# Kernel optimization log

Hardware: AMD Instinct MI355X
Metric: run time of the kernel (lower is better)

Reference implementation:

```python
import jax, jax.numpy as jnp
import numpy as np

N_NODES = 100000
N_EMBED = 64
N_HIDDEN = 64
N_EDGES = 1200000


def setup_inputs() -> dict:
    key = jax.random.key(0)
    ks = jax.random.split(key, 8)
    prop_edge_index = jax.random.randint(ks[0], (2, N_EDGES), 0, N_NODES, dtype=jnp.int64)
    emb = jax.random.normal(ks[1], (N_NODES, N_EMBED), dtype=jnp.float32) * 0.05
    # ChebConv K=2 -> two linear weights per layer + bias
    W1_0 = jax.random.normal(ks[2], (N_EMBED, N_HIDDEN), dtype=jnp.float32) * 0.05
    W1_1 = jax.random.normal(ks[3], (N_EMBED, N_HIDDEN), dtype=jnp.float32) * 0.05
    b1 = jnp.zeros((N_HIDDEN,), dtype=jnp.float32)
    W2_0 = jax.random.normal(ks[4], (N_HIDDEN, N_HIDDEN), dtype=jnp.float32) * 0.05
    W2_1 = jax.random.normal(ks[5], (N_HIDDEN, N_HIDDEN), dtype=jnp.float32) * 0.05
    b2 = jnp.zeros((N_HIDDEN,), dtype=jnp.float32)
    return {"prop_edge_index": prop_edge_index, "emb": emb,
            "W1_0": W1_0, "W1_1": W1_1, "b1": b1,
            "W2_0": W2_0, "W2_1": W2_1, "b2": b2}


def _cheb_norm(edge_index, num_nodes):
    """PyG ChebConv.__norm__ with sym normalization, lambda_max=2.0.
    L_hat = 2L/lambda_max - I = (I - D^-1/2 A D^-1/2) - I, so the net
    diagonal weight is 0 and off-diagonal weight is -d_i^-1/2 * d_j^-1/2.
    Self loops in the input are removed first (weight 0)."""
    row, col = edge_index[0], edge_index[1]
    w = jnp.where(row != col, 1.0, 0.0).astype(jnp.float32)  # remove_self_loops
    deg = jax.ops.segment_sum(w, row, num_segments=num_nodes)
    dinv = jnp.where(deg > 0, deg ** -0.5, 0.0)
    norm = -dinv[row] * w * dinv[col]
    return norm


def _cheb_conv(x, src, dst, norm, W0, W1, b, num_nodes):
    # K=2: out = T0(x) @ W0 + T1(x) @ W1 + b, T0 = x, T1 = L_hat x
    Tx1 = jax.ops.segment_sum(norm[:, None] * x[src], dst, num_segments=num_nodes)
    return x @ W0 + Tx1 @ W1 + b


def reference(prop_edge_index, emb, W1_0, W1_1, b1, W2_0, W2_1, b2):
    src, dst = prop_edge_index[0], prop_edge_index[1]
    norm = _cheb_norm(prop_edge_index, N_NODES)
    x = _cheb_conv(emb, src, dst, norm, W1_0, W1_1, b1, N_NODES)
    x = jax.nn.relu(x)
    # dropout: eval mode (identity)
    x = _cheb_conv(x, src, dst, norm, W2_0, W2_1, b2, N_NODES)
    return x
```

## Files before the change

### kernel.cpp

```cpp
#include <hip/hip_runtime.h>

#define N_NODES 100000
#define N_EDGES 1200000
#define NF 64

typedef __attribute__((ext_vector_type(8))) short short8;
typedef __attribute__((ext_vector_type(4))) float float4v;

__device__ __forceinline__ ushort f2bf(float f) {
    unsigned u = __float_as_uint(f);
    return (ushort)((u + 0x7FFF + ((u >> 16) & 1)) >> 16);
}

#define NBINS 391
#define CAP 4352
#define EPB 2048
#define NBLK 586
#define NI4 (N_EDGES / 4)

#define OFF_CNT    0
#define OFF_ENDP   400128
#define OFF_DINV   800256
#define OFF_CUR    1200384
#define OFF_PKW    1203584
#define OFF_SRCS   1236352
#define OFF_SBIN   8042880
#define OFF_DBIN   11446144
#define OFF_EMBBF  18252672
#define OFF_HBF    31052672

__global__ __launch_bounds__(256) void prepsort(const float* __restrict__ W10,
                                                const float* __restrict__ W11,
                                                const float* __restrict__ W20,
                                                const float* __restrict__ W21,
                                                ushort* __restrict__ pk,
                                                const float* __restrict__ emb,
                                                ushort* __restrict__ emb_bf,
                                                const int* __restrict__ row,
                                                const int* __restrict__ col,
                                                int* __restrict__ cur,
                                                ushort* __restrict__ sbinned,
                                                int* __restrict__ dbinned) {
    int b = blockIdx.x;
    int t = threadIdx.x;
    if (b < NBLK) {
        __shared__ int sh[NBINS], dh[NBINS];
        __shared__ int sbase[NBINS], dbase[NBINS];
        for (int i = t; i < NBINS; i += 256) { sh[i] = 0; dh[i] = 0; }
        __syncthreads();
        int i40 = (b * (EPB / 4)) + t * 2;
        int4 r0 = make_int4(-1, -1, -1, -1), c0 = r0, r1 = r0, c1 = r0;
        if (i40 < NI4)     { r0 = ((const int4*)row)[i40];     c0 = ((const int4*)col)[i40]; }
        if (i40 + 1 < NI4) { r1 = ((const int4*)row)[i40 + 1]; c1 = ((const int4*)col)[i40 + 1]; }
        int s_[8] = {r0.x, r0.y, r0.z, r0.w, r1.x, r1.y, r1.z, r1.w};
        int d_[8] = {c0.x, c0.y, c0.z, c0.w, c1.x, c1.y, c1.z, c1.w};
#pragma unroll
        for (int j = 0; j < 8; ++j)
            if (s_[j] >= 0 && s_[j] != d_[j]) {
                atomicAdd(&sh[s_[j] >> 8], 1);
                atomicAdd(&dh[d_[j] >> 8], 1);
            }
        __syncthreads();
        for (int i = t; i < NBINS; i += 256) {
            if (sh[i]) sbase[i] = i * CAP + atomicAdd(&cur[i], sh[i]);
            if (dh[i]) dbase[i] = i * CAP + atomicAdd(&cur[NBINS + i], dh[i]);
        }
        __syncthreads();
#pragma unroll
        for (int j = 0; j < 8; ++j) {
            int s = s_[j], d = d_[j];
            if (s >= 0 && s != d) {
                int ss = atomicAdd(&sbase[s >> 8], 1);
                sbinned[ss] = (ushort)(s & 255);
                int ds = atomicAdd(&dbase[d >> 8], 1);
                dbinned[ds] = (s << 8) | (d & 255);
            }
        }
    } else if (b < NBLK + 8) {
        int idx = (b - NBLK) * 256 + t;
        int layer = idx >> 10;
        int rest = idx & 1023;
        int f = rest >> 6, L = rest & 63;
        int n = (f & 3) * 16 + (L & 15);
        int kb = (f >> 2) * 32 + ((L >> 4) << 3);
#pragma unroll
        for (int j = 0; j < 8; ++j) {
            int k = kb + j;
            const float* W = layer ? ((k < 64) ? W20 : W21) : ((k < 64) ? W10 : W11);
            pk[idx * 8 + j] = f2bf(W[(k & 63) * 64 + n]);
        }
    } else {
        int bb = b - NBLK - 8;
        int i = (bb * 256 + t) * 8;
        float4 v0 = *(const float4*)(emb + i);
        float4 v1 = *(const float4*)(emb + i + 4);
        uint4 o;
        o.x = (uint)f2bf(v0.x) | ((uint)f2bf(v0.y) << 16);
        o.y = (uint)f2bf(v0.z) | ((uint)f2bf(v0.w) << 16);
        o.z = (uint)f2bf(v1.x) | ((uint)f2bf(v1.y) << 16);
        o.w = (uint)f2bf(v1.z) | ((uint)f2bf(v1.w) << 16);
        *(uint4*)(emb_bf + i) = o;
    }
}

__global__ __launch_bounds__(256) void build(const ushort* __restrict__ sbinned,
                                             const int* __restrict__ dbinned,
                                             const int* __restrict__ cur,
                                             float* __restrict__ dinv,
                                             int* __restrict__ cnt,
                                             int* __restrict__ endp,
                                             int* __restrict__ srcs) {
    int t = threadIdx.x;
    int b = blockIdx.x;
    if (b < NBINS) {
        __shared__ int hist[256];
        hist[t] = 0;
        __syncthreads();
        int start = b * CAP;
        int end = start + cur[b];
        for (int i = start + t; i < end; i += 256)
            atomicAdd(&hist[sbinned[i]], 1);
        __syncthreads();
        int n0 = (b << 8) + t;
        if (n0 < N_NODES) dinv[n0] = hist[t] ? rsqrtf((float)hist[t]) : 0.0f;
    } else {
        int bb = b - NBINS;
        __shared__ int ecache[CAP];
        __shared__ int hist[256];
        __shared__ int lcur[256];
        __shared__ int tot_s;
        hist[t] = 0;
        __syncthreads();
        int start = bb * CAP;
        int len = cur[NBINS + bb];
        for (int i = t; i < len; i += 256) {
            int p = dbinned[start + i];
            ecache[i] = p;
            atomicAdd(&hist[p & 255], 1);
        }
        __syncthreads();
        int o0 = hist[t];
        int A0 = (o0 + 3) & ~3;
        __syncthreads();
        hist[t] = A0;
        __syncthreads();
        for (int off = 1; off < 256; off <<= 1) {
            int v = (t >= off) ? hist[t - off] : 0;
            __syncthreads();
            hist[t] += v;
            __syncthreads();
        }
        int e0 = hist[t] - A0;
        if (t == 255) tot_s = hist[255];
        lcur[t] = start + e0;
        int n0 = (bb << 8) + t;
        if (n0 < N_NODES) { cnt[n0] = o0; endp[n0] = start + e0 + o0; }
        __syncthreads();
        for (int i = t; i < len; i += 256) {
            int p = ecache[i];
            int slot = atomicAdd(&lcur[p & 255], 1);
            srcs[slot] = p >> 8;
        }
        __syncthreads();
        for (int k = o0; k < A0; ++k) srcs[start + e0 + k] = 0;
        if (t < 16) srcs[start + tot_s + t] = 0;
    }
}

#define NPW 16
#define WPB 2
#define NPB (NPW * WPB)
#define LB2 ((N_NODES + NPB - 1) / NPB)

__global__ __launch_bounds__(128, 8) void cheb_layer(const ushort* __restrict__ x,
                                                     const int* __restrict__ srcs,
                                                     const float* __restrict__ dinv,
                                                     const int* __restrict__ endp,
                                                     const int* __restrict__ cnt,
                                                     const ushort* __restrict__ pk,
                                                     const float* __restrict__ bias,
                                                     ushort* __restrict__ out_bf,
                                                     float* __restrict__ out_f32,
                                                     int last) {
    __shared__ ushort sA[WPB][16][136];

    int t = threadIdx.x;
    int lane = t & 63, wid = t >> 6;
    int c = lane & 15, q = lane >> 4;
    int qd = q, fg = c;
    int nb = blockIdx.x * NPB + wid * NPW;

    int nend = 0, ncnt = 0;
    if (lane < NPW && nb + lane < N_NODES) {
        nend = endp[nb + lane];
        ncnt = cnt[nb + lane];
    }

    const uint2* xr = (const uint2*)x;

    auto chunk8 = [&](int eb, int eendL, float& a0, float& a1, float& a2, float& a3) {
        int4 sv = *(const int4*)(srcs + eb);
        int4 sw = *(const int4*)(srcs + eb + 4);
        int sA01 = (qd & 1) ? sv.y : sv.x;
        int sA23 = (qd & 1) ? sv.w : sv.z;
        int srcA = (qd & 2) ? sA23 : sA01;
        int sB01 = (qd & 1) ? sw.y : sw.x;
        int sB23 = (qd & 1) ? sw.w : sw.z;
        int srcB = (qd & 2) ? sB23 : sB01;
        float nAf = dinv[srcA];
        float nBf = dinv[srcB];
        nAf = (eb + qd < eendL) ? nAf : 0.0f;
        nBf = (eb + 4 + qd < eendL) ? nBf : 0.0f;
        uint2 gA = xr[(size_t)srcA * 16 + fg];
        uint2 gB = xr[(size_t)srcB * 16 + fg];
        a0 = fmaf(nAf, __uint_as_float(gA.x << 16), a0);
        a1 = fmaf(nAf, __uint_as_float(gA.x & 0xffff0000u), a1);
        a2 = fmaf(nAf, __uint_as_float(gA.y << 16), a2);
        a3 = fmaf(nAf, __uint_as_float(gA.y & 0xffff0000u), a3);
        a0 = fmaf(nBf, __uint_as_float(gB.x << 16), a0);
        a1 = fmaf(nBf, __uint_as_float(gB.x & 0xffff0000u), a1);
        a2 = fmaf(nBf, __uint_as_float(gB.y << 16), a2);
        a3 = fmaf(nBf, __uint_as_float(gB.y & 0xffff0000u), a3);
    };

#pragma unroll
    for (int gp = 0; gp < NPW; gp += 2) {
        int cn0 = __builtin_amdgcn_readlane(ncnt, gp);
        int ee0 = __builtin_amdgcn_readlane(nend, gp);
        int cn1 = __builtin_amdgcn_readlane(ncnt, gp + 1);
        int ee1 = __builtin_amdgcn_readlane(nend, gp + 1);
        int s0 = ee0 - cn0, s1 = ee1 - cn1;
        float a0 = 0, a1 = 0, a2 = 0, a3 = 0;
        float b0 = 0, b1 = 0, b2 = 0, b3 = 0;

        chunk8(s0,     ee0, a0, a1, a2, a3);
        chunk8(s1,     ee1, b0, b1, b2, b3);
        chunk8(s0 + 8, ee0, a0, a1, a2, a3);
        chunk8(s1 + 8, ee1, b0, b1, b2, b3);
        for (int e = s0 + 16; e < ee0; e += 8) chunk8(e, ee0, a0, a1, a2, a3);
        for (int e = s1 + 16; e < ee1; e += 8) chunk8(e, ee1, b0, b1, b2, b3);

        a0 += __shfl_xor(a0, 16, 64); b0 += __shfl_xor(b0, 16, 64);
        a1 += __shfl_xor(a1, 16, 64); b1 += __shfl_xor(b1, 16, 64);
        a2 += __shfl_xor(a2, 16, 64); b2 += __shfl_xor(b2, 16, 64);
        a3 += __shfl_xor(a3, 16, 64); b3 += __shfl_xor(b3, 16, 64);
        a0 += __shfl_xor(a0, 32, 64); b0 += __shfl_xor(b0, 32, 64);
        a1 += __shfl_xor(a1, 32, 64); b1 += __shfl_xor(b1, 32, 64);
        a2 += __shfl_xor(a2, 32, 64); b2 += __shfl_xor(b2, 32, 64);
        a3 += __shfl_xor(a3, 32, 64); b3 += __shfl_xor(b3, 32, 64);

        int node0 = nb + gp, node1 = nb + gp + 1;
        int ni0 = (node0 < N_NODES) ? node0 : 0;
        int ni1 = (node1 < N_NODES) ? node1 : 0;
        if (qd == 0) {
            uint2 xv0 = xr[(size_t)ni0 * 16 + fg];
            uint2 xv1 = xr[(size_t)ni1 * 16 + fg];
            *(uint2*)&sA[wid][gp][4 * fg] = xv0;
            *(uint2*)&sA[wid][gp + 1][4 * fg] = xv1;
        }
        if (qd == 1) {
            float sc0 = -dinv[ni0];
            float sc1 = -dinv[ni1];
            uint2 p0, p1;
            p0.x = (uint)f2bf(a0 * sc0) | ((uint)f2bf(a1 * sc0) << 16);
            p0.y = (uint)f2bf(a2 * sc0) | ((uint)f2bf(a3 * sc0) << 16);
            p1.x = (uint)f2bf(b0 * sc1) | ((uint)f2bf(b1 * sc1) << 16);
            p1.y = (uint)f2bf(b2 * sc1) | ((uint)f2bf(b3 * sc1) << 16);
            *(uint2*)&sA[wid][gp][64 + 4 * fg] = p0;
            *(uint2*)&sA[wid][gp + 1][64 + 4 * fg] = p1;
        }
    }
    __builtin_amdgcn_wave_barrier();

    const short8* pk8 = (const short8*)pk;
    float4v C[4];
#pragma unroll
    for (int nt = 0; nt < 4; ++nt) {
        float b = bias[nt * 16 + c];
        C[nt] = (float4v){b, b, b, b};
    }
#pragma unroll
    for (int kt = 0; kt < 4; ++kt) {
        short8 af = *(const short8*)&sA[wid][c][kt * 32 + q * 8];
#pragma unroll
        for (int nt = 0; nt < 4; ++nt) {
            short8 bfr = pk8[(kt * 4 + nt) * 64 + lane];
            C[nt] = __builtin_amdgcn_mfma_f32_16x16x32_bf16(af, bfr, C[nt], 0, 0, 0);
        }
    }

#pragma unroll
    for (int nt = 0; nt < 4; ++nt) {
#pragma unroll
        for (int i = 0; i < 4; ++i) {
            int node = nb + q * 4 + i;
            if (node < N_NODES) {
                float v = C[nt][i];
                if (!last) {
                    v = fmaxf(v, 0.0f);
                    out_bf[(size_t)node * NF + nt * 16 + c] = f2bf(v);
                } else {
                    out_f32[(size_t)node * NF + nt * 16 + c] = v;
                }
            }
        }
    }
}

extern "C" void kernel_launch(void* const* d_in, const int* in_sizes, int n_in,
                              void* d_out, int out_size, void* d_ws, size_t ws_size,
                              hipStream_t stream) {
    const int* ei = (const int*)d_in[0];
    const int* row = ei;
    const int* col = ei + N_EDGES;
    const float* emb = (const float*)d_in[1];
    const float* W1_0 = (const float*)d_in[2];
    const float* W1_1 = (const float*)d_in[3];
    const float* b1 = (const float*)d_in[4];
    const float* W2_0 = (const float*)d_in[5];
    const float* W2_1 = (const float*)d_in[6];
    const float* b2 = (const float*)d_in[7];
    float* out = (float*)d_out;

    char* ws = (char*)d_ws;
    int* cnt = (int*)(ws + OFF_CNT);
    int* endp = (int*)(ws + OFF_ENDP);
    float* dinv = (float*)(ws + OFF_DINV);
    int* cur = (int*)(ws + OFF_CUR);
    ushort* pk = (ushort*)(ws + OFF_PKW);
    int* srcs = (int*)(ws + OFF_SRCS);
    ushort* sbinned = (ushort*)(ws + OFF_SBIN);
    int* dbinned = (int*)(ws + OFF_DBIN);
    ushort* emb_bf = (ushort*)(ws + OFF_EMBBF);
    ushort* h_bf = (ushort*)(ws + OFF_HBF);

    hipMemsetAsync(cur, 0, 2 * NBINS * sizeof(int), stream);
    prepsort<<<NBLK + 8 + 3125, 256, 0, stream>>>(W1_0, W1_1, W2_0, W2_1, pk,
                                                  emb, emb_bf, row, col, cur,
                                                  sbinned, dbinned);
    build<<<2 * NBINS, 256, 0, stream>>>(sbinned, dbinned, cur, dinv, cnt, endp, srcs);

    cheb_layer<<<LB2, 128, 0, stream>>>(emb_bf, srcs, dinv, endp, cnt, pk, b1, h_bf, nullptr, 0);
    cheb_layer<<<LB2, 128, 0, stream>>>(h_bf, srcs, dinv, endp, cnt, pk + 8192, b2, nullptr, out, 1);
}
```

Baseline: 213.8 us.

## Stage binned edges in LDS before coalesced global writes in sort kernels

The binning kernel now uses 512-thread blocks with twice the edges per block. It computes per-block bin offsets with a prefix scan, scatters edges into shared-memory staging buffers, and then writes each bin's run contiguously to global memory instead of doing random per-edge global scatter. The build kernel likewise assembles its CSR source list in shared memory and writes it out linearly, re-reading dbinned instead of caching it. The goal is to cut uncoalesced scattered global writes, at the cost of more LDS use, an extra scan and more barriers, which may reduce occupancy.

Result: faster. 187.2 us (-12.4%).

```diff
diff --git a/kernel.cpp b/kernel.cpp
--- a/kernel.cpp
+++ b/kernel.cpp
@@ -14,8 +14,8 @@
 
 #define NBINS 391
 #define CAP 4352
-#define EPB 2048
-#define NBLK 586
+#define EPB 4096
+#define NBLK 293
 #define NI4 (N_EDGES / 4)
 
 #define OFF_CNT    0
@@ -29,7 +29,7 @@
 #define OFF_EMBBF  18252672
 #define OFF_HBF    31052672
 
-__global__ __launch_bounds__(256) void prepsort(const float* __restrict__ W10,
+__global__ __launch_bounds__(512) void prepsort(const float* __restrict__ W10,
                                                 const float* __restrict__ W11,
                                                 const float* __restrict__ W20,
                                                 const float* __restrict__ W21,
@@ -45,10 +45,16 @@
     int t = threadIdx.x;
     if (b < NBLK) {
         __shared__ int sh[NBINS], dh[NBINS];
-        __shared__ int sbase[NBINS], dbase[NBINS];
-        for (int i = t; i < NBINS; i += 256) { sh[i] = 0; dh[i] = 0; }
-        __syncthreads();
-        int i40 = (b * (EPB / 4)) + t * 2;
+        __shared__ int sst[NBINS], dstt[NBINS];
+        __shared__ int sgb[NBINS], dgb[NBINS];
+        __shared__ int slc[NBINS], dlc[NBINS];
+        __shared__ int ssc[512], dsc[512];
+        __shared__ ushort sloc[EPB];
+        __shared__ int dloc[EPB];
+        __shared__ ushort sbid[EPB], dbid[EPB];
+        for (int i = t; i < NBINS; i += 512) { sh[i] = 0; dh[i] = 0; }
+        __syncthreads();
+        int i40 = b * (EPB / 4) + t * 2;
         int4 r0 = make_int4(-1, -1, -1, -1), c0 = r0, r1 = r0, c1 = r0;
         if (i40 < NI4)     { r0 = ((const int4*)row)[i40];     c0 = ((const int4*)col)[i40]; }
         if (i40 + 1 < NI4) { r1 = ((const int4*)row)[i40 + 1]; c1 = ((const int4*)col)[i40 + 1]; }
@@ -61,23 +67,50 @@
                 atomicAdd(&dh[d_[j] >> 8], 1);
             }
         __syncthreads();
-        for (int i = t; i < NBINS; i += 256) {
-            if (sh[i]) sbase[i] = i * CAP + atomicAdd(&cur[i], sh[i]);
-            if (dh[i]) dbase[i] = i * CAP + atomicAdd(&cur[NBINS + i], dh[i]);
+        int cs = 0, cd = 0;
+        if (t < NBINS) {
+            cs = sh[t]; cd = dh[t];
+            sgb[t] = t * CAP + atomicAdd(&cur[t], cs);
+            dgb[t] = t * CAP + atomicAdd(&cur[NBINS + t], cd);
+        }
+        ssc[t] = (t < NBINS) ? cs : 0;
+        dsc[t] = (t < NBINS) ? cd : 0;
+        __syncthreads();
+        for (int off = 1; off < 512; off <<= 1) {
+            int vs = 0, vd = 0;
+            if (t >= off) { vs = ssc[t - off]; vd = dsc[t - off]; }
+            __syncthreads();
+            ssc[t] += vs; dsc[t] += vd;
+            __syncthreads();
+        }
+        if (t < NBINS) {
+            sst[t] = ssc[t] - cs; slc[t] = sst[t];
+            dstt[t] = dsc[t] - cd; dlc[t] = dstt[t];
         }
         __syncthreads();
 #pragma unroll
         for (int j = 0; j < 8; ++j) {
             int s = s_[j], d = d_[j];
             if (s >= 0 && s != d) {
-                int ss = atomicAdd(&sbase[s >> 8], 1);
-                sbinned[ss] = (ushort)(s & 255);
-                int ds = atomicAdd(&dbase[d >> 8], 1);
-                dbinned[ds] = (s << 8) | (d & 255);
+                int sb = s >> 8, db = d >> 8;
+                int ls = atomicAdd(&slc[sb], 1);
+                sloc[ls] = (ushort)(s & 255); sbid[ls] = (ushort)sb;
+                int ld = atomicAdd(&dlc[db], 1);
+                dloc[ld] = (s << 8) | (d & 255); dbid[ld] = (ushort)db;
             }
         }
-    } else if (b < NBLK + 8) {
-        int idx = (b - NBLK) * 256 + t;
+        __syncthreads();
+        int totS = ssc[511], totD = dsc[511];
+        for (int i = t; i < totS; i += 512) {
+            int bi = sbid[i];
+            sbinned[sgb[bi] + (i - sst[bi])] = sloc[i];
+        }
+        for (int i = t; i < totD; i += 512) {
+            int bi = dbid[i];
+            dbinned[dgb[bi] + (i - dstt[bi])] = dloc[i];
+        }
+    } else if (b < NBLK + 4) {
+        int idx = (b - NBLK) * 512 + t;
         int layer = idx >> 10;
         int rest = idx & 1023;
         int f = rest >> 6, L = rest & 63;
@@ -90,16 +123,18 @@
             pk[idx * 8 + j] = f2bf(W[(k & 63) * 64 + n]);
         }
     } else {
-        int bb = b - NBLK - 8;
-        int i = (bb * 256 + t) * 8;
-        float4 v0 = *(const float4*)(emb + i);
-        float4 v1 = *(const float4*)(emb + i + 4);
-        uint4 o;
-        o.x = (uint)f2bf(v0.x) | ((uint)f2bf(v0.y) << 16);
-        o.y = (uint)f2bf(v0.z) | ((uint)f2bf(v0.w) << 16);
-        o.z = (uint)f2bf(v1.x) | ((uint)f2bf(v1.y) << 16);
-        o.w = (uint)f2bf(v1.z) | ((uint)f2bf(v1.w) << 16);
-        *(uint4*)(emb_bf + i) = o;
+        int bb = b - NBLK - 4;
+        int i = (bb * 512 + t) * 8;
+        if (i < N_NODES * NF) {
+            float4 v0 = *(const float4*)(emb + i);
+            float4 v1 = *(const float4*)(emb + i + 4);
+            uint4 o;
+            o.x = (uint)f2bf(v0.x) | ((uint)f2bf(v0.y) << 16);
+            o.y = (uint)f2bf(v0.z) | ((uint)f2bf(v0.w) << 16);
+            o.z = (uint)f2bf(v1.x) | ((uint)f2bf(v1.y) << 16);
+            o.w = (uint)f2bf(v1.z) | ((uint)f2bf(v1.w) << 16);
+            *(uint4*)(emb_bf + i) = o;
+        }
     }
 }
 
@@ -117,27 +152,24 @@
         hist[t] = 0;
         __syncthreads();
         int start = b * CAP;
-        int end = start + cur[b];
-        for (int i = start + t; i < end; i += 256)
-            atomicAdd(&hist[sbinned[i]], 1);
+        int len = cur[b];
+        for (int i = t; i < len; i += 256)
+            atomicAdd(&hist[sbinned[start + i]], 1);
         __syncthreads();
         int n0 = (b << 8) + t;
         if (n0 < N_NODES) dinv[n0] = hist[t] ? rsqrtf((float)hist[t]) : 0.0f;
     } else {
         int bb = b - NBINS;
-        __shared__ int ecache[CAP];
         __shared__ int hist[256];
         __shared__ int lcur[256];
+        __shared__ int obuf[CAP];
         __shared__ int tot_s;
         hist[t] = 0;
         __syncthreads();
         int start = bb * CAP;
         int len = cur[NBINS + bb];
-        for (int i = t; i < len; i += 256) {
-            int p = dbinned[start + i];
-            ecache[i] = p;
-            atomicAdd(&hist[p & 255], 1);
-        }
+        for (int i = t; i < len; i += 256)
+            atomicAdd(&hist[dbinned[start + i] & 255], 1);
         __syncthreads();
         int o0 = hist[t];
         int A0 = (o0 + 3) & ~3;
@@ -152,18 +184,21 @@
         }
         int e0 = hist[t] - A0;
         if (t == 255) tot_s = hist[255];
-        lcur[t] = start + e0;
+        lcur[t] = e0;
         int n0 = (bb << 8) + t;
         if (n0 < N_NODES) { cnt[n0] = o0; endp[n0] = start + e0 + o0; }
         __syncthreads();
         for (int i = t; i < len; i += 256) {
-            int p = ecache[i];
+            int p = dbinned[start + i];
             int slot = atomicAdd(&lcur[p & 255], 1);
-            srcs[slot] = p >> 8;
-        }
-        __syncthreads();
-        for (int k = o0; k < A0; ++k) srcs[start + e0 + k] = 0;
-        if (t < 16) srcs[start + tot_s + t] = 0;
+            obuf[slot] = p >> 8;
+        }
+        for (int k = o0; k < A0; ++k) obuf[e0 + k] = 0;
+        __syncthreads();
+        if (t < 16) obuf[tot_s + t] = 0;
+        __syncthreads();
+        int tot = tot_s + 16;
+        for (int i = t; i < tot; i += 256) srcs[start + i] = obuf[i];
     }
 }
 
@@ -335,7 +370,7 @@
     ushort* h_bf = (ushort*)(ws + OFF_HBF);
 
     hipMemsetAsync(cur, 0, 2 * NBINS * sizeof(int), stream);
-    prepsort<<<NBLK + 8 + 3125, 256, 0, stream>>>(W1_0, W1_1, W2_0, W2_1, pk,
+    prepsort<<<NBLK + 4 + 1563, 512, 0, stream>>>(W1_0, W1_1, W2_0, W2_1, pk,
                                                   emb, emb_bf, row, col, cur,
                                                   sbinned, dbinned);
     build<<<2 * NBINS, 256, 0, stream>>>(sbinned, dbinned, cur, dinv, cnt, endp, srcs);
```
